# Kernel optimization log

Measured on AMD Instinct MI355X. Metric: run time of the kernel, lower is better.

## Reference

```python
import jax, jax.numpy as jnp
import numpy as np
from functools import partial

EPS = 1e-5
CHANS = [(3, 64), (64, 64), (64, 128), (128, 128), (128, 256), (256, 256), (256, 256), (256, 256)]

def conv3d(x, w):
    # x: [B,X,Y,Z,Cin], w: [3,3,3,Cin,Cout]; Minkowski stride-1 conv keeps coords -> SAME padding
    return jax.lax.conv_general_dilated(x, w, window_strides=(1, 1, 1), padding='SAME',
                                        dimension_numbers=('NDHWC', 'DHWIO', 'NDHWC'))

def bn(x, g, b):
    # training-mode batch norm over all voxels (MinkowskiBatchNorm forward)
    m = jnp.mean(x, axis=(0, 1, 2, 3))
    v = jnp.var(x, axis=(0, 1, 2, 3))
    return (x - m) * jax.lax.rsqrt(v + EPS) * g + b

def maxpool2(x):
    return jax.lax.reduce_window(x, -jnp.inf, jax.lax.max,
                                 (1, 2, 2, 2, 1), (1, 2, 2, 2, 1), 'VALID')

def setup_inputs() -> dict:
    key = jax.random.key(0)
    ks = jax.random.split(key, 32)
    inp = {'x': jax.random.normal(ks[0], (2, 64, 64, 64, 3), dtype=jnp.float32)}
    for i, (ci, co) in enumerate(CHANS):
        scale = (2.0 / (27 * ci)) ** 0.5  # kaiming for 3x3x3 conv
        inp[f'w{i+1}'] = jax.random.normal(ks[1 + i], (3, 3, 3, ci, co), dtype=jnp.float32) * scale
        inp[f'g{i+1}'] = jnp.ones((co,), dtype=jnp.float32)
        inp[f'b{i+1}'] = jnp.zeros((co,), dtype=jnp.float32)
    inp['wl'] = jax.random.normal(ks[20], (256, 256), dtype=jnp.float32) * (1.0 / 16.0)
    inp['bl'] = jnp.zeros((256,), dtype=jnp.float32)
    return inp

def reference(x, w1, g1, b1, w2, g2, b2, w3, g3, b3, w4, g4, b4,
              w5, g5, b5, w6, g6, b6, w7, g7, b7, w8, g8, b8, wl, bl):
    h = jax.nn.relu(bn(conv3d(x, w1), g1, b1))
    h = jax.nn.relu(bn(conv3d(h, w2), g2, b2))
    h = maxpool2(h)                                   # 64 -> 32
    h = jax.nn.relu(bn(conv3d(h, w3), g3, b3))
    h = jax.nn.relu(bn(conv3d(h, w4), g4, b4))
    h = maxpool2(h)                                   # 32 -> 16
    h = jax.nn.relu(bn(conv3d(h, w5), g5, b5))
    h = jax.nn.relu(bn(conv3d(h, w6), g6, b6))
    h = jax.nn.relu(bn(conv3d(h, w7), g7, b7))
    h = maxpool2(h)                                   # 16 -> 8
    h = bn(conv3d(h, w8), g8, b8)                     # no ReLU before global pool in source
    h = jnp.mean(h, axis=(1, 2, 3))                   # MinkowskiGlobalPooling (avg over coords)
    return h @ wl + bl                                # MinkowskiLinear(256, out_feat)
```

## Files before the change

### kernel.cpp

```cpp
#include <hip/hip_runtime.h>


typedef _Float16 f16;
typedef _Float16 f16x8 __attribute__((ext_vector_type(8)));
typedef float f32x4 __attribute__((ext_vector_type(4)));

struct WArgs {
  const float* src[8];
  int end[8];
  int S[8], G[8], CR[8], CO[8];
};
__global__ __launch_bounds__(256) void wprep_all(WArgs a, f16* __restrict__ wf)
{
  const int e = blockIdx.x * 256 + threadIdx.x;
  int li = 0;
  while (li < 7 && e >= a.end[li]) ++li;
  if (e >= a.end[li]) return;
  const int base = li ? a.end[li - 1] : 0;
  int x = e - base;
  const int i = x & 7;
  const int l = (x >> 3) & 63;
  int r = x >> 9;
  const int g = r % a.G[li]; r /= a.G[li];
  const int s = r % a.S[li]; r /= a.S[li];
  const int t = r;
  const int k = s * 32 + ((l >> 4) << 3) + i;
  const int co = g * 16 + (l & 15);
  const float v = (k < a.CR[li]) ? a.src[li][((long)t * a.CR[li] + k) * a.CO[li] + co] : 0.f;
  wf[e] = (f16)v;
}

template<int CIN, int CINR, int Z, int WR, int WC, bool HASBN, int SS>
__global__ __launch_bounds__(WR*WC*64) void conv_mfma(
    const float* __restrict__ xin, const f16* __restrict__ wf,
    float* __restrict__ out, int X, int Y, int Co,
    const float* __restrict__ sc, const float* __restrict__ sh,
    float* __restrict__ part, int partBase,
    float* __restrict__ pout, long outE)
{
  constexpr int NTHR = WR * WC * 64;
  constexpr int L = 64 * WR / Z;
  constexpr int RB = (CIN + 8) * 2;
  constexpr int S = CIN / 32;
  constexpr int COW = 64 * WC;
  constexpr bool SPLIT = (SS > 0);
  __shared__ __align__(16) char slab[(L + 2) * (Z + 2) * RB];
  __shared__ float sstat[WR * WC][2][64];

  const int tid = threadIdx.x;
  const int lane = tid & 63;
  const int wv = tid >> 6;
  const int wr = wv / WC, wc = wv % WC;

  const long vb = (long)blockIdx.x * (64 * WR);
  const int XYZ = X * Y * Z;
  const int n = (int)(vb / XYZ);
  const int rem = (int)(vb % XYZ);
  const int x0 = rem / (Y * Z);
  const int y0 = (rem % (Y * Z)) / Z;
  const int co0 = blockIdx.y * COW;
  const int Gtot = Co >> 4;
  const int g0 = (co0 >> 4) + wc * 4;

  int abase[4];
  #pragma unroll
  for (int r = 0; r < 4; ++r) {
    const int vl = wr * 64 + r * 16 + (lane & 15);
    const int ly = vl / Z, z = vl % Z;
    abase[r] = (ly * (Z + 2) + z) * RB + ((lane >> 4) << 4);
  }

  f32x4 acc[4][4];
  const f32x4 fz = {0.f, 0.f, 0.f, 0.f};
  #pragma unroll
  for (int r = 0; r < 4; ++r)
    #pragma unroll
    for (int c = 0; c < 4; ++c) acc[r][c] = fz;

  {
    const f16x8 hz = {};
    for (int e = tid * 8; e < (L + 2) * 2 * CIN; e += NTHR * 8) {
      const int pr = e / CIN, ci = e % CIN;
      const int row = (pr >> 1) * (Z + 2) + (pr & 1) * (Z + 1);
      *(f16x8*)(slab + row * RB + ci * 2) = hz;
    }
  }

  auto stage = [&](int dx) {
    const int xs = x0 + dx - 1;
    const bool xok = (xs >= 0) && (xs < X);
    const long gv0 = ((long)(n * X + xs) * Y + (y0 - 1)) * Z;
    if constexpr (CINR == CIN) {
      constexpr int NE = (L + 2) * Z * CIN;
      for (int e = tid * 8; e < NE; e += NTHR * 8) {
        const int rr = e / CIN, ci = e % CIN;
        const int li = rr / Z, z = rr % Z;
        const int ys = y0 - 1 + li;
        f16x8 h = {};
        if (xok && ys >= 0 && ys < Y) {
          const float* p = xin + (gv0 + rr) * CIN + ci;
          float4 v0 = *(const float4*)p;
          float4 v1 = *(const float4*)(p + 4);
          if constexpr (HASBN) {
            const float4 s0 = *(const float4*)(sc + ci);
            const float4 s1 = *(const float4*)(sc + ci + 4);
            const float4 h0 = *(const float4*)(sh + ci);
            const float4 h1 = *(const float4*)(sh + ci + 4);
            v0.x = fmaxf(fmaf(v0.x, s0.x, h0.x), 0.f);
            v0.y = fmaxf(fmaf(v0.y, s0.y, h0.y), 0.f);
            v0.z = fmaxf(fmaf(v0.z, s0.z, h0.z), 0.f);
            v0.w = fmaxf(fmaf(v0.w, s0.w, h0.w), 0.f);
            v1.x = fmaxf(fmaf(v1.x, s1.x, h1.x), 0.f);
            v1.y = fmaxf(fmaf(v1.y, s1.y, h1.y), 0.f);
            v1.z = fmaxf(fmaf(v1.z, s1.z, h1.z), 0.f);
            v1.w = fmaxf(fmaf(v1.w, s1.w, h1.w), 0.f);
          }
          h[0] = (f16)v0.x; h[1] = (f16)v0.y; h[2] = (f16)v0.z; h[3] = (f16)v0.w;
          h[4] = (f16)v1.x; h[5] = (f16)v1.y; h[6] = (f16)v1.z; h[7] = (f16)v1.w;
        }
        *(f16x8*)(slab + (li * (Z + 2) + 1 + z) * RB + ci * 2) = h;
      }
    } else {
      for (int rr = tid; rr < (L + 2) * Z; rr += NTHR) {
        const int li = rr / Z, z = rr % Z;
        const int ys = y0 - 1 + li;
        f16x8 h = {};
        if (xok && ys >= 0 && ys < Y) {
          const float* p = xin + (gv0 + rr) * CINR;
          #pragma unroll
          for (int i = 0; i < CINR; ++i) h[i] = (f16)p[i];
        }
        char* drow = slab + (li * (Z + 2) + 1 + z) * RB;
        *(f16x8*)drow = h;
        const f16x8 hz = {};
        #pragma unroll
        for (int ch = 1; ch < CIN / 8; ++ch) *(f16x8*)(drow + ch * 16) = hz;
      }
    }
  };

  auto ktaps = [&](int dx, int s) {
    #pragma unroll
    for (int dy = 0; dy < 3; ++dy) {
      #pragma unroll
      for (int dzi = 0; dzi < 3; ++dzi) {
        f16x8 av[4];
        #pragma unroll
        for (int r = 0; r < 4; ++r)
          av[r] = *(const f16x8*)(slab + abase[r] + s * 64 + (dy * (Z + 2) + dzi) * RB);
        const int t = dx * 9 + dy * 3 + dzi;
        f16x8 bv[4];
        #pragma unroll
        for (int c = 0; c < 4; ++c)
          bv[c] = *(const f16x8*)((const char*)wf +
                    (((long)(t * S + s) * Gtot + g0 + c) << 10) + (lane << 4));
        #pragma unroll
        for (int r = 0; r < 4; ++r)
          #pragma unroll
          for (int c = 0; c < 4; ++c)
            acc[r][c] = __builtin_amdgcn_mfma_f32_16x16x32_f16(av[r], bv[c], acc[r][c], 0, 0, 0);
      }
    }
  };

  if constexpr (SPLIT) {
    constexpr int SCH = S / SS;
    const int zb = blockIdx.z;
    const int dx = zb / SS;
    const int s0 = (zb % SS) * SCH;
    stage(dx);
    __syncthreads();
    #pragma unroll
    for (int si = 0; si < SCH; ++si) ktaps(dx, s0 + si);
  } else {
    for (int dx = 0; dx < 3; ++dx) {
      __syncthreads();
      stage(dx);
      __syncthreads();
      for (int s = 0; s < S; ++s) ktaps(dx, s);
    }
  }

  const long vgbase = vb + wr * 64;
  const int cobase = co0 + wc * 64;
  if constexpr (SPLIT) {
    float* pb = pout + (long)blockIdx.z * outE;
    #pragma unroll
    for (int r = 0; r < 4; ++r)
      #pragma unroll
      for (int c = 0; c < 4; ++c)
        #pragma unroll
        for (int q = 0; q < 4; ++q) {
          const long vox = vgbase + r * 16 + ((lane >> 4) << 2) + q;
          const int co = cobase + c * 16 + (lane & 15);
          pb[vox * Co + co] = acc[r][c][q];
        }
    return;
  }

  #pragma unroll
  for (int r = 0; r < 4; ++r)
    #pragma unroll
    for (int c = 0; c < 4; ++c)
      #pragma unroll
      for (int q = 0; q < 4; ++q) {
        const long vox = vgbase + r * 16 + ((lane >> 4) << 2) + q;
        const int co = cobase + c * 16 + (lane & 15);
        out[vox * Co + co] = acc[r][c][q];
      }

  float s4[4], q4[4];
  #pragma unroll
  for (int c = 0; c < 4; ++c) {
    float s = 0.f, q = 0.f;
    #pragma unroll
    for (int r = 0; r < 4; ++r)
      #pragma unroll
      for (int qd = 0; qd < 4; ++qd) {
        const float v = acc[r][c][qd];
        s += v;
        q = fmaf(v, v, q);
      }
    s4[c] = s; q4[c] = q;
  }
  #pragma unroll
  for (int c = 0; c < 4; ++c) {
    s4[c] += __shfl_xor(s4[c], 16);
    s4[c] += __shfl_xor(s4[c], 32);
    q4[c] += __shfl_xor(q4[c], 16);
    q4[c] += __shfl_xor(q4[c], 32);
  }
  if (lane < 16) {
    #pragma unroll
    for (int c = 0; c < 4; ++c) {
      sstat[wv][0][c * 16 + lane] = s4[c];
      sstat[wv][1][c * 16 + lane] = q4[c];
    }
  }
  __syncthreads();
  const long entry = (long)blockIdx.y * gridDim.x + blockIdx.x + partBase;
  for (int t = tid; t < WC * 128; t += NTHR) {
    const int wcc = t >> 7, k = (t >> 6) & 1, ch = t & 63;
    float v = 0.f;
    #pragma unroll
    for (int wr2 = 0; wr2 < WR; ++wr2) v += sstat[wr2 * WC + wcc][k][ch];
    part[entry * (2 * COW) + k * COW + wcc * 64 + ch] = v;
  }
}

__global__ __launch_bounds__(256) void reduce_stats(
    const float* __restrict__ pout, float* __restrict__ out,
    long outE, int KS, int vpb, float* __restrict__ part)
{
  const int tid = threadIdx.x;
  const int wv = tid >> 6, lane = tid & 63;
  const int vbase = blockIdx.x * vpb;
  float4 s = {0.f, 0.f, 0.f, 0.f}, q = {0.f, 0.f, 0.f, 0.f};
  for (int v = vbase + wv; v < vbase + vpb; v += 4) {
    const long e = (long)v * 256 + lane * 4;
    float4 o = *(const float4*)(pout + e);
    for (int z = 1; z < KS; ++z) {
      const float4 p = *(const float4*)(pout + (long)z * outE + e);
      o.x += p.x; o.y += p.y; o.z += p.z; o.w += p.w;
    }
    *(float4*)(out + e) = o;
    s.x += o.x; s.y += o.y; s.z += o.z; s.w += o.w;
    q.x = fmaf(o.x, o.x, q.x); q.y = fmaf(o.y, o.y, q.y);
    q.z = fmaf(o.z, o.z, q.z); q.w = fmaf(o.w, o.w, q.w);
  }
  __shared__ float st[4][2][256];
  *(float4*)&st[wv][0][lane * 4] = s;
  *(float4*)&st[wv][1][lane * 4] = q;
  __syncthreads();
  for (int t = tid; t < 512; t += 256) {
    const int k = t >> 8, ch = t & 255;
    part[(long)blockIdx.x * 512 + k * 256 + ch] =
        st[0][k][ch] + st[1][k][ch] + st[2][k][ch] + st[3][k][ch];
  }
}

__global__ __launch_bounds__(256) void stats_final(
    const float* __restrict__ part, int nbx, int CoWin, long nvox,
    const float* __restrict__ g, const float* __restrict__ b,
    float* __restrict__ sc, float* __restrict__ sh)
{
  const int c = blockIdx.x;
  const int by = c / CoWin;
  const int cw = c % CoWin;
  const int tid = threadIdx.x;
  float s = 0.f, ss = 0.f;
  for (int i = tid; i < nbx; i += 256) {
    const long base = ((long)by * nbx + i) * 2 * CoWin;
    s += part[base + cw];
    ss += part[base + CoWin + cw];
  }
  __shared__ float r0[256];
  __shared__ float r1[256];
  r0[tid] = s; r1[tid] = ss;
  __syncthreads();
  #pragma unroll
  for (int o = 128; o > 0; o >>= 1) {
    if (tid < o) { r0[tid] += r0[tid + o]; r1[tid] += r1[tid + o]; }
    __syncthreads();
  }
  if (tid == 0) {
    const float inv = 1.f / (float)nvox;
    const float m = r0[0] * inv;
    const float var = r1[0] * inv - m * m;
    const float scale = rsqrtf(var + 1e-5f) * g[c];
    sc[c] = scale;
    sh[c] = b[c] - m * scale;
  }
}

__global__ __launch_bounds__(256) void maxpool2_aff(
    const float* __restrict__ in, float* __restrict__ out,
    int N, int X, int Y, int Z, int C,
    const float* __restrict__ sc, const float* __restrict__ sh)
{
  const int OX = X >> 1, OY = Y >> 1, OZ = Z >> 1;
  const int c4n = C >> 2;
  const long nout = (long)N * OX * OY * OZ * c4n;
  long idx = (long)blockIdx.x * 256 + threadIdx.x;
  if (idx >= nout) return;
  const int c4 = (int)(idx % c4n);
  long v = idx / c4n;
  const int oz = (int)(v % OZ); v /= OZ;
  const int oy = (int)(v % OY); v /= OY;
  const int ox = (int)(v % OX);
  const int n = (int)(v / OX);
  const long sx = (long)Y * Z * C, sy = (long)Z * C, sz = C;
  const long base = ((((long)n * X + 2 * ox) * Y + 2 * oy) * Z + 2 * oz) * (long)C + 4L * c4;
  float4 m = *reinterpret_cast<const float4*>(in + base);
  #pragma unroll
  for (int dd = 1; dd < 8; ++dd) {
    const int dxp = dd >> 2, dyp = (dd >> 1) & 1, dzp = dd & 1;
    const float4 t = *reinterpret_cast<const float4*>(in + base + dxp * sx + dyp * sy + dzp * sz);
    m.x = fmaxf(m.x, t.x); m.y = fmaxf(m.y, t.y);
    m.z = fmaxf(m.z, t.z); m.w = fmaxf(m.w, t.w);
  }
  const int c = 4 * c4;
  const float4 s4 = *reinterpret_cast<const float4*>(sc + c);
  const float4 h4 = *reinterpret_cast<const float4*>(sh + c);
  m.x = fmaxf(fmaf(m.x, s4.x, h4.x), 0.f);
  m.y = fmaxf(fmaf(m.y, s4.y, h4.y), 0.f);
  m.z = fmaxf(fmaf(m.z, s4.z, h4.z), 0.f);
  m.w = fmaxf(fmaf(m.w, s4.w, h4.w), 0.f);
  *reinterpret_cast<float4*>(out + idx * 4) = m;
}

__global__ __launch_bounds__(256) void head_mean(
    const float* __restrict__ x8, const float* __restrict__ sc, const float* __restrict__ sh,
    float* __restrict__ hbuf)
{
  const int n = blockIdx.x, cg = blockIdx.y;
  const int tx = threadIdx.x & 63, ty = threadIdx.x >> 6;
  const int c = cg * 64 + tx;
  float s = 0.f;
  for (int v = ty; v < 512; v += 4) s += x8[((long)n * 512 + v) * 256 + c];
  __shared__ float red[4][64];
  red[ty][tx] = s;
  __syncthreads();
  if (ty == 0) {
    s = red[0][tx] + red[1][tx] + red[2][tx] + red[3][tx];
    hbuf[n * 256 + c] = fmaf(s * (1.f / 512.f), sc[c], sh[c]);
  }
}

__global__ __launch_bounds__(256) void head_mv(
    const float* __restrict__ hbuf, const float* __restrict__ wl,
    const float* __restrict__ bl, float* __restrict__ out)
{
  const int n = blockIdx.x, og = blockIdx.y;
  const int tx = threadIdx.x & 63, ty = threadIdx.x >> 6;
  const int oc = og * 64 + tx;
  float a = 0.f;
  const int k0 = ty * 64;
  for (int k = k0; k < k0 + 64; ++k)
    a = fmaf(hbuf[n * 256 + k], wl[(long)k * 256 + oc], a);
  __shared__ float red[4][64];
  red[ty][tx] = a;
  __syncthreads();
  if (ty == 0)
    out[n * 256 + oc] = red[0][tx] + red[1][tx] + red[2][tx] + red[3][tx] + bl[oc];
}

extern "C" void kernel_launch(void* const* d_in, const int* in_sizes, int n_in,
                              void* d_out, int out_size, void* d_ws, size_t ws_size,
                              hipStream_t stream)
{
  const float* x = (const float*)d_in[0];
  const float* W[8];
  const float* G[8];
  const float* B[8];
  for (int i = 0; i < 8; ++i) {
    W[i] = (const float*)d_in[1 + 3 * i];
    G[i] = (const float*)d_in[2 + 3 * i];
    B[i] = (const float*)d_in[3 + 3 * i];
  }
  const float* wl = (const float*)d_in[25];
  const float* bl = (const float*)d_in[26];

  float* A    = (float*)d_ws;
  float* Bb   = A + 33554432L;
  float* part = Bb + 16777216L;
  float* scb  = part + 262144L;
  float* shb  = scb + 2048L;
  float* hbuf = shb + 2048L;
  f16*   wfb  = (f16*)(hbuf + 512L);

  const int wfS[8]  = {1, 2, 2, 4, 4, 8, 8, 8};
  const int wfG[8]  = {4, 4, 8, 8, 16, 16, 16, 16};
  const int wfCR[8] = {3, 64, 64, 128, 128, 256, 256, 256};
  const int wfCO[8] = {64, 64, 128, 128, 256, 256, 256, 256};
  long wfOff[9];
  wfOff[0] = 0;
  for (int i = 0; i < 8; ++i) wfOff[i + 1] = wfOff[i] + 27L * wfS[i] * wfG[i] * 512;
  if (ws_size < (size_t)((char*)(wfb + wfOff[8]) - (char*)d_ws)) return;
  auto WF = [&](int i) { return wfb + wfOff[i]; };
  auto SC = [&](int i) { return scb + i * 256; };
  auto SH = [&](int i) { return shb + i * 256; };

  {
    WArgs a;
    for (int i = 0; i < 8; ++i) {
      a.src[i] = W[i]; a.end[i] = (int)wfOff[i + 1];
      a.S[i] = wfS[i]; a.G[i] = wfG[i]; a.CR[i] = wfCR[i]; a.CO[i] = wfCO[i];
    }
    wprep_all<<<(unsigned)((wfOff[8] + 255) / 256), 256, 0, stream>>>(a, wfb);
  }

  auto fin = [&](int layer, int nbx, int CoWin, int C, long nvox) {
    stats_final<<<C, 256, 0, stream>>>(part, nbx, CoWin, nvox,
                                       G[layer], B[layer], SC(layer), SH(layer));
  };
  auto pool_aff = [&](const float* in, float* ob, int N, int Xd, int Yd, int Zd, int C, int layer) {
    const long nout = (long)N * (Xd / 2) * (Yd / 2) * (Zd / 2) * (C / 4);
    maxpool2_aff<<<(unsigned)((nout + 255) / 256), 256, 0, stream>>>(
        in, ob, N, Xd, Yd, Zd, C, SC(layer), SH(layer));
  };

  const long V64 = 262144;
  float* pK = A + 4194304L;

  conv_mfma<32, 3, 64, 4, 1, false, 0><<<dim3(2048, 1), 256, 0, stream>>>(
      x, WF(0), A, 64, 64, 64, nullptr, nullptr, part, 0, nullptr, 0);
  fin(0, 2048, 64, 64, 2 * V64);
  conv_mfma<64, 64, 64, 4, 1, true, 0><<<dim3(1024, 1), 256, 0, stream>>>(
      A, WF(1), Bb, 64, 64, 64, SC(0), SH(0), part, 0, nullptr, 0);
  conv_mfma<64, 64, 64, 4, 1, true, 0><<<dim3(1024, 1), 256, 0, stream>>>(
      A + V64 * 64, WF(1), A, 64, 64, 64, SC(0), SH(0), part, 1024, nullptr, 0);
  fin(1, 2048, 64, 64, 2 * V64);
  {
    float* P = A + 16777216L;
    pool_aff(Bb, P,            1, 64, 64, 64, 64, 1);
    pool_aff(A,  P + 2097152L, 1, 64, 64, 64, 64, 1);
  }

  const float* P1 = A + 16777216L;
  conv_mfma<64, 64, 32, 2, 2, false, 0><<<dim3(512, 1), 256, 0, stream>>>(
      P1, WF(2), A, 32, 32, 128, nullptr, nullptr, part, 0, nullptr, 0);
  fin(2, 512, 128, 128, 65536);
  conv_mfma<128, 128, 32, 2, 2, true, 0><<<dim3(512, 1), 256, 0, stream>>>(
      A, WF(3), Bb, 32, 32, 128, SC(2), SH(2), part, 0, nullptr, 0);
  fin(3, 512, 128, 128, 65536);
  float* Q = Bb + 8388608L;
  pool_aff(Bb, Q, 2, 32, 32, 32, 128, 3);

  const long E16 = 2097152;
  conv_mfma<128, 128, 16, 1, 4, false, 1><<<dim3(128, 1, 3), 256, 0, stream>>>(
      Q, WF(4), nullptr, 16, 16, 256, nullptr, nullptr, nullptr, 0, pK, E16);
  reduce_stats<<<256, 256, 0, stream>>>(pK, A, E16, 3, 32, part);
  fin(4, 256, 256, 256, 8192);
  conv_mfma<256, 256, 16, 1, 4, true, 1><<<dim3(128, 1, 3), 256, 0, stream>>>(
      A, WF(5), nullptr, 16, 16, 256, SC(4), SH(4), nullptr, 0, pK, E16);
  reduce_stats<<<256, 256, 0, stream>>>(pK, Bb, E16, 3, 32, part);
  fin(5, 256, 256, 256, 8192);
  conv_mfma<256, 256, 16, 1, 4, true, 1><<<dim3(128, 1, 3), 256, 0, stream>>>(
      Bb, WF(6), nullptr, 16, 16, 256, SC(5), SH(5), nullptr, 0, pK, E16);
  reduce_stats<<<256, 256, 0, stream>>>(pK, A + E16, E16, 3, 32, part);
  fin(6, 256, 256, 256, 8192);
  float* R = A;
  pool_aff(A + E16, R, 2, 16, 16, 16, 256, 6);

  const long E8 = 262144;
  conv_mfma<256, 256, 8, 1, 4, false, 4><<<dim3(16, 1, 12), 256, 0, stream>>>(
      R, WF(7), nullptr, 8, 8, 256, nullptr, nullptr, nullptr, 0, pK, E8);
  reduce_stats<<<256, 256, 0, stream>>>(pK, Bb, E8, 12, 4, part);
  fin(7, 256, 256, 256, 1024);

  head_mean<<<dim3(2, 4), 256, 0, stream>>>(Bb, SC(7), SH(7), hbuf);
  head_mv<<<dim3(2, 4), 256, 0, stream>>>(hbuf, wl, bl, (float*)d_out);
}
```

Baseline: 627.4 us.

## Store intermediate activations in fp16 and swizzle conv blocks across XCDs

```diff
diff --git a/kernel.cpp b/kernel.cpp
--- a/kernel.cpp
+++ b/kernel.cpp
@@ -3,7 +3,14 @@
 
 typedef _Float16 f16;
 typedef _Float16 f16x8 __attribute__((ext_vector_type(8)));
+typedef _Float16 f16x4 __attribute__((ext_vector_type(4)));
 typedef float f32x4 __attribute__((ext_vector_type(4)));
+
+__device__ __forceinline__ int xcd_swz(int bx, int nbx) {
+  const int q = nbx >> 3, r = nbx & 7;
+  const int x = bx & 7, o = bx >> 3;
+  return (x < r ? x * (q + 1) : r * (q + 1) + (x - r) * q) + o;
+}
 
 struct WArgs {
   const float* src[8];
@@ -32,8 +39,8 @@
 
 template<int CIN, int CINR, int Z, int WR, int WC, bool HASBN, int SS>
 __global__ __launch_bounds__(WR*WC*64) void conv_mfma(
-    const float* __restrict__ xin, const f16* __restrict__ wf,
-    float* __restrict__ out, int X, int Y, int Co,
+    const void* __restrict__ xin, const f16* __restrict__ wf,
+    f16* __restrict__ out, int X, int Y, int Co,
     const float* __restrict__ sc, const float* __restrict__ sh,
     float* __restrict__ part, int partBase,
     float* __restrict__ pout, long outE)
@@ -52,7 +59,8 @@
   const int wv = tid >> 6;
   const int wr = wv / WC, wc = wv % WC;
 
-  const long vb = (long)blockIdx.x * (64 * WR);
+  const int bxs = xcd_swz(blockIdx.x, gridDim.x);
+  const long vb = (long)bxs * (64 * WR);
   const int XYZ = X * Y * Z;
   const int n = (int)(vb / XYZ);
   const int rem = (int)(vb % XYZ);
@@ -91,6 +99,7 @@
     const bool xok = (xs >= 0) && (xs < X);
     const long gv0 = ((long)(n * X + xs) * Y + (y0 - 1)) * Z;
     if constexpr (CINR == CIN) {
+      const f16* xf = (const f16*)xin;
       constexpr int NE = (L + 2) * Z * CIN;
       for (int e = tid * 8; e < NE; e += NTHR * 8) {
         const int rr = e / CIN, ci = e % CIN;
@@ -98,35 +107,34 @@
         const int ys = y0 - 1 + li;
         f16x8 h = {};
         if (xok && ys >= 0 && ys < Y) {
-          const float* p = xin + (gv0 + rr) * CIN + ci;
-          float4 v0 = *(const float4*)p;
-          float4 v1 = *(const float4*)(p + 4);
+          const f16x8 hv = *(const f16x8*)(xf + (gv0 + rr) * CIN + ci);
           if constexpr (HASBN) {
             const float4 s0 = *(const float4*)(sc + ci);
             const float4 s1 = *(const float4*)(sc + ci + 4);
             const float4 h0 = *(const float4*)(sh + ci);
             const float4 h1 = *(const float4*)(sh + ci + 4);
-            v0.x = fmaxf(fmaf(v0.x, s0.x, h0.x), 0.f);
-            v0.y = fmaxf(fmaf(v0.y, s0.y, h0.y), 0.f);
-            v0.z = fmaxf(fmaf(v0.z, s0.z, h0.z), 0.f);
-            v0.w = fmaxf(fmaf(v0.w, s0.w, h0.w), 0.f);
-            v1.x = fmaxf(fmaf(v1.x, s1.x, h1.x), 0.f);
-            v1.y = fmaxf(fmaf(v1.y, s1.y, h1.y), 0.f);
-            v1.z = fmaxf(fmaf(v1.z, s1.z, h1.z), 0.f);
-            v1.w = fmaxf(fmaf(v1.w, s1.w, h1.w), 0.f);
+            h[0] = (f16)fmaxf(fmaf((float)hv[0], s0.x, h0.x), 0.f);
+            h[1] = (f16)fmaxf(fmaf((float)hv[1], s0.y, h0.y), 0.f);
+            h[2] = (f16)fmaxf(fmaf((float)hv[2], s0.z, h0.z), 0.f);
+            h[3] = (f16)fmaxf(fmaf((float)hv[3], s0.w, h0.w), 0.f);
+            h[4] = (f16)fmaxf(fmaf((float)hv[4], s1.x, h1.x), 0.f);
+            h[5] = (f16)fmaxf(fmaf((float)hv[5], s1.y, h1.y), 0.f);
+            h[6] = (f16)fmaxf(fmaf((float)hv[6], s1.z, h1.z), 0.f);
+            h[7] = (f16)fmaxf(fmaf((float)hv[7], s1.w, h1.w), 0.f);
+          } else {
+            h = hv;
           }
-          h[0] = (f16)v0.x; h[1] = (f16)v0.y; h[2] = (f16)v0.z; h[3] = (f16)v0.w;
-          h[4] = (f16)v1.x; h[5] = (f16)v1.y; h[6] = (f16)v1.z; h[7] = (f16)v1.w;
         }
         *(f16x8*)(slab + (li * (Z + 2) + 1 + z) * RB + ci * 2) = h;
       }
     } else {
+      const float* xf = (const float*)xin;
       for (int rr = tid; rr < (L + 2) * Z; rr += NTHR) {
         const int li = rr / Z, z = rr % Z;
         const int ys = y0 - 1 + li;
         f16x8 h = {};
         if (xok && ys >= 0 && ys < Y) {
-          const float* p = xin + (gv0 + rr) * CINR;
+          const float* p = xf + (gv0 + rr) * CINR;
           #pragma unroll
           for (int i = 0; i < CINR; ++i) h[i] = (f16)p[i];
         }
@@ -206,7 +214,7 @@
       for (int q = 0; q < 4; ++q) {
         const long vox = vgbase + r * 16 + ((lane >> 4) << 2) + q;
         const int co = cobase + c * 16 + (lane & 15);
-        out[vox * Co + co] = acc[r][c][q];
+        out[vox * Co + co] = (f16)acc[r][c][q];
       }
 
   float s4[4], q4[4];
@@ -238,7 +246,7 @@
     }
   }
   __syncthreads();
-  const long entry = (long)blockIdx.y * gridDim.x + blockIdx.x + partBase;
+  const long entry = (long)blockIdx.y * gridDim.x + bxs + partBase;
   for (int t = tid; t < WC * 128; t += NTHR) {
     const int wcc = t >> 7, k = (t >> 6) & 1, ch = t & 63;
     float v = 0.f;
@@ -249,7 +257,7 @@
 }
 
 __global__ __launch_bounds__(256) void reduce_stats(
-    const float* __restrict__ pout, float* __restrict__ out,
+    const float* __restrict__ pout, f16* __restrict__ out,
     long outE, int KS, int vpb, float* __restrict__ part)
 {
   const int tid = threadIdx.x;
@@ -263,7 +271,8 @@
       const float4 p = *(const float4*)(pout + (long)z * outE + e);
       o.x += p.x; o.y += p.y; o.z += p.z; o.w += p.w;
     }
-    *(float4*)(out + e) = o;
+    f16x4 ov = {(f16)o.x, (f16)o.y, (f16)o.z, (f16)o.w};
+    *(f16x4*)(out + e) = ov;
     s.x += o.x; s.y += o.y; s.z += o.z; s.w += o.w;
     q.x = fmaf(o.x, o.x, q.x); q.y = fmaf(o.y, o.y, q.y);
     q.z = fmaf(o.z, o.z, q.z); q.w = fmaf(o.w, o.w, q.w);
@@ -314,7 +323,7 @@
 }
 
 __global__ __launch_bounds__(256) void maxpool2_aff(
-    const float* __restrict__ in, float* __restrict__ out,
+    const f16* __restrict__ in, f16* __restrict__ out,
     int N, int X, int Y, int Z, int C,
     const float* __restrict__ sc, const float* __restrict__ sh)
 {
@@ -331,33 +340,34 @@
   const int n = (int)(v / OX);
   const long sx = (long)Y * Z * C, sy = (long)Z * C, sz = C;
   const long base = ((((long)n * X + 2 * ox) * Y + 2 * oy) * Z + 2 * oz) * (long)C + 4L * c4;
-  float4 m = *reinterpret_cast<const float4*>(in + base);
+  f16x4 m = *(const f16x4*)(in + base);
   #pragma unroll
   for (int dd = 1; dd < 8; ++dd) {
     const int dxp = dd >> 2, dyp = (dd >> 1) & 1, dzp = dd & 1;
-    const float4 t = *reinterpret_cast<const float4*>(in + base + dxp * sx + dyp * sy + dzp * sz);
-    m.x = fmaxf(m.x, t.x); m.y = fmaxf(m.y, t.y);
-    m.z = fmaxf(m.z, t.z); m.w = fmaxf(m.w, t.w);
+    const f16x4 t = *(const f16x4*)(in + base + dxp * sx + dyp * sy + dzp * sz);
+    #pragma unroll
+    for (int i = 0; i < 4; ++i) m[i] = (t[i] > m[i]) ? t[i] : m[i];
   }
   const int c = 4 * c4;
-  const float4 s4 = *reinterpret_cast<const float4*>(sc + c);
-  const float4 h4 = *reinterpret_cast<const float4*>(sh + c);
-  m.x = fmaxf(fmaf(m.x, s4.x, h4.x), 0.f);
-  m.y = fmaxf(fmaf(m.y, s4.y, h4.y), 0.f);
-  m.z = fmaxf(fmaf(m.z, s4.z, h4.z), 0.f);
-  m.w = fmaxf(fmaf(m.w, s4.w, h4.w), 0.f);
-  *reinterpret_cast<float4*>(out + idx * 4) = m;
+  const float4 s4 = *(const float4*)(sc + c);
+  const float4 h4 = *(const float4*)(sh + c);
+  f16x4 r;
+  r[0] = (f16)fmaxf(fmaf((float)m[0], s4.x, h4.x), 0.f);
+  r[1] = (f16)fmaxf(fmaf((float)m[1], s4.y, h4.y), 0.f);
+  r[2] = (f16)fmaxf(fmaf((float)m[2], s4.z, h4.z), 0.f);
+  r[3] = (f16)fmaxf(fmaf((float)m[3], s4.w, h4.w), 0.f);
+  *(f16x4*)(out + idx * 4) = r;
 }
 
 __global__ __launch_bounds__(256) void head_mean(
-    const float* __restrict__ x8, const float* __restrict__ sc, const float* __restrict__ sh,
+    const f16* __restrict__ x8, const float* __restrict__ sc, const float* __restrict__ sh,
     float* __restrict__ hbuf)
 {
   const int n = blockIdx.x, cg = blockIdx.y;
   const int tx = threadIdx.x & 63, ty = threadIdx.x >> 6;
   const int c = cg * 64 + tx;
   float s = 0.f;
-  for (int v = ty; v < 512; v += 4) s += x8[((long)n * 512 + v) * 256 + c];
+  for (int v = ty; v < 512; v += 4) s += (float)x8[((long)n * 512 + v) * 256 + c];
   __shared__ float red[4][64];
   red[ty][tx] = s;
   __syncthreads();
@@ -401,9 +411,11 @@
   const float* wl = (const float*)d_in[25];
   const float* bl = (const float*)d_in[26];
 
-  float* A    = (float*)d_ws;
-  float* Bb   = A + 33554432L;
-  float* part = Bb + 16777216L;
+  char* ws = (char*)d_ws;
+  f16*   A    = (f16*)ws;
+  f16*   Bb   = (f16*)(ws + (64L << 20));
+  float* pK   = (float*)(ws + (128L << 20));
+  float* part = (float*)(ws + (152L << 20));
   float* scb  = part + 262144L;
   float* shb  = scb + 2048L;
   float* hbuf = shb + 2048L;
@@ -416,7 +428,7 @@
   long wfOff[9];
   wfOff[0] = 0;
   for (int i = 0; i < 8; ++i) wfOff[i + 1] = wfOff[i] + 27L * wfS[i] * wfG[i] * 512;
-  if (ws_size < (size_t)((char*)(wfb + wfOff[8]) - (char*)d_ws)) return;
+  if (ws_size < (size_t)((char*)(wfb + wfOff[8]) - ws)) return;
   auto WF = [&](int i) { return wfb + wfOff[i]; };
   auto SC = [&](int i) { return scb + i * 256; };
   auto SH = [&](int i) { return shb + i * 256; };
@@ -434,42 +446,31 @@
     stats_final<<<C, 256, 0, stream>>>(part, nbx, CoWin, nvox,
                                        G[layer], B[layer], SC(layer), SH(layer));
   };
-  auto pool_aff = [&](const float* in, float* ob, int N, int Xd, int Yd, int Zd, int C, int layer) {
+  auto pool_aff = [&](const f16* in, f16* ob, int N, int Xd, int Yd, int Zd, int C, int layer) {
     const long nout = (long)N * (Xd / 2) * (Yd / 2) * (Zd / 2) * (C / 4);
     maxpool2_aff<<<(unsigned)((nout + 255) / 256), 256, 0, stream>>>(
         in, ob, N, Xd, Yd, Zd, C, SC(layer), SH(layer));
   };
 
-  const long V64 = 262144;
-  float* pK = A + 4194304L;
-
   conv_mfma<32, 3, 64, 4, 1, false, 0><<<dim3(2048, 1), 256, 0, stream>>>(
       x, WF(0), A, 64, 64, 64, nullptr, nullptr, part, 0, nullptr, 0);
-  fin(0, 2048, 64, 64, 2 * V64);
-  conv_mfma<64, 64, 64, 4, 1, true, 0><<<dim3(1024, 1), 256, 0, stream>>>(
+  fin(0, 2048, 64, 64, 524288);
+  conv_mfma<64, 64, 64, 4, 1, true, 0><<<dim3(2048, 1), 256, 0, stream>>>(
       A, WF(1), Bb, 64, 64, 64, SC(0), SH(0), part, 0, nullptr, 0);
-  conv_mfma<64, 64, 64, 4, 1, true, 0><<<dim3(1024, 1), 256, 0, stream>>>(
-      A + V64 * 64, WF(1), A, 64, 64, 64, SC(0), SH(0), part, 1024, nullptr, 0);
-  fin(1, 2048, 64, 64, 2 * V64);
-  {
-    float* P = A + 16777216L;
-    pool_aff(Bb, P,            1, 64, 64, 64, 64, 1);
-    pool_aff(A,  P + 2097152L, 1, 64, 64, 64, 64, 1);
-  }
-
-  const float* P1 = A + 16777216L;
+  fin(1, 2048, 64, 64, 524288);
+  pool_aff(Bb, A, 2, 64, 64, 64, 64, 1);
+
   conv_mfma<64, 64, 32, 2, 2, false, 0><<<dim3(512, 1), 256, 0, stream>>>(
-      P1, WF(2), A, 32, 32, 128, nullptr, nullptr, part, 0, nullptr, 0);
+      A, WF(2), Bb, 32, 32, 128, nullptr, nullptr, part, 0, nullptr, 0);
   fin(2, 512, 128, 128, 65536);
   conv_mfma<128, 128, 32, 2, 2, true, 0><<<dim3(512, 1), 256, 0, stream>>>(
-      A, WF(3), Bb, 32, 32, 128, SC(2), SH(2), part, 0, nullptr, 0);
+      Bb, WF(3), A, 32, 32, 128, SC(2), SH(2), part, 0, nullptr, 0);
   fin(3, 512, 128, 128, 65536);
-  float* Q = Bb + 8388608L;
-  pool_aff(Bb, Q, 2, 32, 32, 32, 128, 3);
+  pool_aff(A, Bb, 2, 32, 32, 32, 128, 3);
 
   const long E16 = 2097152;
   conv_mfma<128, 128, 16, 1, 4, false, 1><<<dim3(128, 1, 3), 256, 0, stream>>>(
-      Q, WF(4), nullptr, 16, 16, 256, nullptr, nullptr, nullptr, 0, pK, E16);
+      Bb, WF(4), nullptr, 16, 16, 256, nullptr, nullptr, nullptr, 0, pK, E16);
   reduce_stats<<<256, 256, 0, stream>>>(pK, A, E16, 3, 32, part);
   fin(4, 256, 256, 256, 8192);
   conv_mfma<256, 256, 16, 1, 4, true, 1><<<dim3(128, 1, 3), 256, 0, stream>>>(
@@ -478,17 +479,16 @@
   fin(5, 256, 256, 256, 8192);
   conv_mfma<256, 256, 16, 1, 4, true, 1><<<dim3(128, 1, 3), 256, 0, stream>>>(
       Bb, WF(6), nullptr, 16, 16, 256, SC(5), SH(5), nullptr, 0, pK, E16);
-  reduce_stats<<<256, 256, 0, stream>>>(pK, A + E16, E16, 3, 32, part);
+  reduce_stats<<<256, 256, 0, stream>>>(pK, A, E16, 3, 32, part);
   fin(6, 256, 256, 256, 8192);
-  float* R = A;
-  pool_aff(A + E16, R, 2, 16, 16, 16, 256, 6);
+  pool_aff(A, Bb, 2, 16, 16, 16, 256, 6);
 
   const long E8 = 262144;
   conv_mfma<256, 256, 8, 1, 4, false, 4><<<dim3(16, 1, 12), 256, 0, stream>>>(
-      R, WF(7), nullptr, 8, 8, 256, nullptr, nullptr, nullptr, 0, pK, E8);
-  reduce_stats<<<256, 256, 0, stream>>>(pK, Bb, E8, 12, 4, part);
+      Bb, WF(7), nullptr, 8, 8, 256, nullptr, nullptr, nullptr, 0, pK, E8);
+  reduce_stats<<<256, 256, 0, stream>>>(pK, A, E8, 12, 4, part);
   fin(7, 256, 256, 256, 1024);
 
-  head_mean<<<dim3(2, 4), 256, 0, stream>>>(Bb, SC(7), SH(7), hbuf);
+  head_mean<<<dim3(2, 4), 256, 0, stream>>>(A, SC(7), SH(7), hbuf);
   head_mv<<<dim3(2, 4), 256, 0, stream>>>(hbuf, wl, bl, (float*)d_out);
 }
```

Result: faster. 563.0 us (-10.3%).
